# Kernel optimization log

Hardware: AMD Instinct MI355X
Metric: run time of the kernel (lower is better)

Reference implementation:

```python
import jax, jax.numpy as jnp
import numpy as np

B, S, H = 4, 1024, 2048
E = 16            # num_experts
K = 2             # num_experts_per_token
I = 1024          # per-expert intermediate_dim
N_SHARED = 2
I_SHARED = I * N_SHARED
RATIO = 0.1       # shared_expert_ratio
EPS = 1e-9


def _swiglu(x, wg, wu, wd):
    # SwiGLU, bias=False: down( silu(gate(x)) * up(x) )
    return (jax.nn.silu(x @ wg) * (x @ wu)) @ wd


def setup_inputs() -> dict:
    key = jax.random.key(0)
    ks = jax.random.split(key, 9)
    scale = 0.02
    x = jax.random.normal(ks[0], (B, S, H), dtype=jnp.float32)
    centroids = jax.random.normal(ks[1], (E, H), dtype=jnp.float32)  # nn.Parameter(randn)
    gate_bias = jnp.zeros((E,), dtype=jnp.float32)
    # shared expert SwiGLU weights (intermediate = I * n_shared_experts)
    wg_s = jax.random.normal(ks[2], (H, I_SHARED), dtype=jnp.float32) * scale
    wu_s = jax.random.normal(ks[3], (H, I_SHARED), dtype=jnp.float32) * scale
    wd_s = jax.random.normal(ks[4], (I_SHARED, H), dtype=jnp.float32) * scale
    # routed experts, stacked [E, ...]
    wg = jax.random.normal(ks[5], (E, H, I), dtype=jnp.float32) * scale
    wu = jax.random.normal(ks[6], (E, H, I), dtype=jnp.float32) * scale
    wd = jax.random.normal(ks[7], (E, I, H), dtype=jnp.float32) * scale
    return {"x": x, "centroids": centroids, "gate_bias": gate_bias,
            "wg_s": wg_s, "wu_s": wu_s, "wd_s": wd_s,
            "wg": wg, "wu": wu, "wd": wd}


def reference(x, centroids, gate_bias, wg_s, wu_s, wd_s, wg, wu, wd):
    # 1) shared expert on ALL tokens, scaled by ratio
    shared = _swiglu(x, wg_s, wu_s, wd_s) * RATIO          # [B,S,H]
    # 2) centroid affinity (DeepSeek-V3 sigmoid gating)
    affinity = jax.nn.sigmoid(jnp.einsum('bsh,eh->bse', x, centroids))  # [B,S,E]
    # 3) bias used ONLY for selection
    biased = affinity + gate_bias
    _, top_idx = jax.lax.top_k(biased, K)                  # [B,S,K]
    # 4) clean weights from unbiased affinity, normalized to sum 1
    top_aff = jnp.take_along_axis(affinity, top_idx, axis=-1)  # [B,S,K]
    weights = top_aff / (top_aff.sum(-1, keepdims=True) + EPS)
    # 5) combine-mask: per-token per-expert weight (0 if not selected)
    mask = (jax.nn.one_hot(top_idx, E, dtype=x.dtype) * weights[..., None]).sum(-2)  # [B,S,E]
    # 6) expert compute + weighted combine; loop over fixed small E avoids
    #    materializing a [B,S,E,H] tensor
    routed = jnp.zeros_like(x)
    for e in range(E):
        routed = routed + mask[..., e:e + 1] * _swiglu(x, wg[e], wu[e], wd[e])
    return shared + routed
```

## Files before the change

kernel.cpp:

```cpp
#include <hip/hip_runtime.h>
#include <hip/hip_bf16.h>

typedef unsigned short u16;
typedef unsigned int u32;
typedef unsigned long long u64;
typedef __attribute__((ext_vector_type(8))) short short8;
typedef __attribute__((ext_vector_type(4))) float f32x4;

#define TOKENS 4096
#define HDIM 2048
#define NEXP 16
#define IDIM 1024
#define ISH 2048
#define NCHUNK 128

#define GUITEMS 1152
#define DITEMS 2048

#define AS1(p) ((const __attribute__((address_space(1))) u32*)(p))
#define AS3(p) ((__attribute__((address_space(3))) u32*)(p))

__device__ __forceinline__ u16 f2b(float f) {
    u32 u = __float_as_uint(f);
    u32 r = u + 0x7fffu + ((u >> 16) & 1u);
    return (u16)(r >> 16);
}

__device__ __forceinline__ int item_index(int bid) {
    int x = bid & 7, j = bid >> 3;
    return ((x + 8 * (j >> 4)) << 4) | (j & 15);
}

__global__ __launch_bounds__(256) void route_kernel(const float* __restrict__ x,
                                                    const float* __restrict__ cent,
                                                    const float* __restrict__ bias,
                                                    u16* __restrict__ xb,
                                                    int* __restrict__ top_e,
                                                    float* __restrict__ top_w) {
    __shared__ alignas(16) float cs[8 * 2048];
    int lane = threadIdx.x & 63;
    int wv = threadIdx.x >> 6;
    int t = blockIdx.x * 4 + wv;
    const float4* xp4 = (const float4*)(x + (size_t)t * HDIM);
    float4 xr[8];
#pragma unroll
    for (int i = 0; i < 8; i++) xr[i] = xp4[lane + 64 * i];
    u16* xbp = xb + (size_t)t * HDIM;
#pragma unroll
    for (int i = 0; i < 8; i++) {
        u32 lo = (u32)f2b(xr[i].x) | ((u32)f2b(xr[i].y) << 16);
        u32 hi = (u32)f2b(xr[i].z) | ((u32)f2b(xr[i].w) << 16);
        uint2 o = make_uint2(lo, hi);
        *(uint2*)(xbp + (size_t)(lane + 64 * i) * 4) = o;
    }
    float aff[16];
#pragma unroll
    for (int ph = 0; ph < 2; ph++) {
        if (ph) __syncthreads();
        const float* sbase = cent + (size_t)(ph * 8 + wv * 2) * HDIM;
        float* dbase = cs + (size_t)wv * 2 * HDIM;
#pragma unroll
        for (int i = 0; i < 16; i++) {
            __builtin_amdgcn_global_load_lds(AS1(sbase + i * 256 + lane * 4),
                                             AS3(dbase + i * 256), 16, 0, 0);
        }
        __syncthreads();
#pragma unroll
        for (int e = 0; e < 8; e++) {
            const float4* cp = (const float4*)cs + (size_t)e * 512;
            float s = 0.f;
#pragma unroll
            for (int i = 0; i < 8; i++) {
                float4 cv = cp[lane + 64 * i];
                s += xr[i].x * cv.x;
                s += xr[i].y * cv.y;
                s += xr[i].z * cv.z;
                s += xr[i].w * cv.w;
            }
#pragma unroll
            for (int off = 32; off > 0; off >>= 1) s += __shfl_xor(s, off, 64);
            aff[ph * 8 + e] = 1.f / (1.f + expf(-s));
        }
    }
    float b0 = -1e30f, b1 = -1e30f, a0 = 0.f, a1 = 0.f;
    int e0 = -1, e1 = -1;
#pragma unroll
    for (int e = 0; e < 16; e++) {
        float v = aff[e] + bias[e];
        if (v > b0) {
            b1 = b0; e1 = e0; a1 = a0;
            b0 = v; e0 = e; a0 = aff[e];
        } else if (v > b1) {
            b1 = v; e1 = e; a1 = aff[e];
        }
    }
    float inv = 1.f / (a0 + a1 + 1e-9f);
    if (lane == 0) {
        top_e[2 * t] = e0; top_w[2 * t] = a0 * inv;
        top_e[2 * t + 1] = e1; top_w[2 * t + 1] = a1 * inv;
    }
}

__global__ __launch_bounds__(1024) void build_kernel(
    const int* __restrict__ top_e, const float* __restrict__ top_w,
    int* __restrict__ counts, int* __restrict__ offsets, int* __restrict__ itemsGU,
    int* __restrict__ itemsD, int* __restrict__ list_tok, int* __restrict__ tok2slot) {
    __shared__ int cnt[NCHUNK][16];
    __shared__ int offs_s[16];
    __shared__ int totals[16];
    __shared__ int guPref[16], dPref[16];
    int tid = threadIdx.x;
    int lane = tid & 63, wv = tid >> 6;
    for (int i = tid; i < GUITEMS; i += 1024) itemsGU[i] = -1;
    for (int i = tid; i < DITEMS; i += 1024) itemsD[i] = -1;
    for (int c = wv; c < NCHUNK; c += 16) {
        int v = top_e[c * 64 + lane];
#pragma unroll
        for (int e = 0; e < 16; e++) {
            u64 m = __ballot(v == e);
            if (lane == 0) cnt[c][e] = (int)__popcll(m);
        }
    }
    __syncthreads();
    if (tid < 16) {
        int s = 0;
        for (int c = 0; c < NCHUNK; c++) s += cnt[c][tid];
        totals[tid] = s;
        counts[tid] = s;
    }
    __syncthreads();
    if (tid == 0) {
        int r = 0, g = 0, d = 0;
        for (int e = 0; e < 16; e++) {
            offs_s[e] = r;
            offsets[e] = r;
            r += totals[e];
            guPref[e] = g;
            g += ((totals[e] + 127) >> 7) * 8;
            dPref[e] = d;
            d += ((totals[e] + 255) >> 8) * 32;
        }
    }
    if (tid < 512) {
        int i = tid;
        int g = i >> 4, s = i & 15;
        int y0 = (g >> 3) << 2, m0 = (g & 7) << 2;
        itemsGU[i] = ((m0 + (s >> 2)) << 8) | (y0 + (s & 3));
    }
    if (tid < 512) {
        int i = tid;
        int g = i >> 4, s = i & 15;
        int y0 = (g >> 2) << 2, m0 = (g & 3) << 2;
        itemsD[i] = ((m0 + (s >> 2)) << 8) | (y0 + (s & 3));
    }
    __syncthreads();
    if (tid < 16) {
        int e = tid;
        int tA = (totals[e] + 127) >> 7;
        int p = 512 + guPref[e];
        for (int y0 = 0; y0 < 8; y0 += 4)
            for (int m = 0; m < tA; m++)
                for (int dy = 0; dy < 4; dy++)
                    itemsGU[p++] = (1 << 28) | (e << 20) | (m << 8) | (y0 + dy);
        int tB = (totals[e] + 255) >> 8;
        p = 512 + dPref[e];
        for (int y0 = 0; y0 < 32; y0 += 4)
            for (int m = 0; m < tB; m++)
                for (int dy = 0; dy < 4; dy++)
                    itemsD[p++] = (1 << 28) | (e << 20) | (m << 8) | (y0 + dy);
        int r = offs_s[e];
        for (int c = 0; c < NCHUNK; c++) {
            int v = cnt[c][e];
            cnt[c][e] = r;
            r += v;
        }
    }
    __syncthreads();
    for (int c = wv; c < NCHUNK; c += 16) {
        int i = c * 64 + lane;
        int v = top_e[i];
        int rank = 0;
#pragma unroll
        for (int e = 0; e < 16; e++) {
            u64 m = __ballot(v == e);
            if (v == e) rank = (int)__popcll(m & ((1ull << lane) - 1ull));
        }
        int slot = cnt[c][v] + rank;
        list_tok[slot] = i >> 1;
        tok2slot[i] = slot;
    }
}

__global__ __launch_bounds__(256) void conv_all_kernel(
    const float* __restrict__ wgs, const float* __restrict__ wus,
    const float* __restrict__ wds, const float* __restrict__ wg,
    const float* __restrict__ wu, const float* __restrict__ wd, u16* __restrict__ Wt_gs,
    u16* __restrict__ Wt_us, u16* __restrict__ Wt_ds, u16* __restrict__ Wt_g,
    u16* __restrict__ Wt_u, u16* __restrict__ Wt_d) {
    int id = blockIdx.x;
    const float* Wm;
    u16* Wtm;
    int K, N, nt, kc;
    if (id < 768) {
        K = 2048; N = 2048;
        int seg = id >> 8, r = id & 255;
        nt = r & 31; kc = r >> 5;
        if (seg == 0) { Wm = wgs; Wtm = Wt_gs; }
        else if (seg == 1) { Wm = wus; Wtm = Wt_us; }
        else { Wm = wds; Wtm = Wt_ds; }
    } else if (id < 4864) {
        K = 2048; N = 1024;
        int r = id - 768;
        int m = r >> 11;
        r &= 2047;
        int e = r >> 7;
        r &= 127;
        nt = r & 15; kc = r >> 4;
        size_t off = (size_t)e * 2048 * 1024;
        if (m == 0) { Wm = wg + off; Wtm = Wt_g + off; }
        else { Wm = wu + off; Wtm = Wt_u + off; }
    } else {
        K = 1024; N = 2048;
        int r = id - 4864;
        int e = r >> 7;
        r &= 127;
        nt = r & 31; kc = r >> 5;
        size_t off = (size_t)e * 1024 * 2048;
        Wm = wd + off; Wtm = Wt_d + off;
    }
    int ksB = K >> 5;
    __shared__ u16 Ls[64 * 40];
    int t = threadIdx.x;
    int kr = t >> 3, ng = t & 7;
    int nn = t >> 2, seg2 = t & 3;
    int g = seg2 ^ ((nn >> 2) & 3);
#pragma unroll
    for (int s = 0; s < 8; s++) {
        int kb = kc * 256 + s * 32;
        const float* src = Wm + (size_t)(kb + kr) * N + nt * 64 + ng * 8;
        float4 f0 = *(const float4*)src;
        float4 f1 = *(const float4*)(src + 4);
        __syncthreads();
        const float* p0 = (const float*)&f0;
        const float* p1 = (const float*)&f1;
#pragma unroll
        for (int l = 0; l < 4; l++) Ls[(8 * ng + l) * 40 + kr] = f2b(p0[l]);
#pragma unroll
        for (int l = 0; l < 4; l++) Ls[(8 * ng + 4 + l) * 40 + kr] = f2b(p1[l]);
        __syncthreads();
        const u16* lp = &Ls[nn * 40 + g * 8];
        u32 w0 = (u32)lp[0] | ((u32)lp[1] << 16);
        u32 w1 = (u32)lp[2] | ((u32)lp[3] << 16);
        u32 w2 = (u32)lp[4] | ((u32)lp[5] << 16);
        u32 w3 = (u32)lp[6] | ((u32)lp[7] << 16);
        uint4 o = make_uint4(w0, w1, w2, w3);
        *(uint4*)(Wtm + (size_t)(nt * ksB + (kb >> 5)) * 2048 + t * 8) = o;
    }
}

__global__ __launch_bounds__(512, 4) void gemm_gateup(
    const u16* __restrict__ A, const u16* __restrict__ BgS, const u16* __restrict__ BuS,
    const u16* __restrict__ BgR, const u16* __restrict__ BuR, u16* __restrict__ hS,
    u16* __restrict__ hR, const int* __restrict__ counts, const int* __restrict__ offsets,
    const int* __restrict__ list_tok, const int* __restrict__ items) {
    int it = items[item_index(blockIdx.x)];
    if (it < 0) return;
    int routed = (it >> 28) & 1;
    int e = (it >> 20) & 15;
    int m0 = ((it >> 8) & 4095) * 128;
    int yb = it & 255;
    int cnt, base, Nout;
    u16* hout;
    const u16 *BgBase, *BuBase;
    if (routed) {
        cnt = counts[e];
        base = offsets[e];
        Nout = IDIM;
        size_t off = (size_t)e * HDIM * IDIM;
        BgBase = BgR + off;
        BuBase = BuR + off;
        hout = hR;
    } else {
        cnt = TOKENS;
        base = 0;
        Nout = ISH;
        BgBase = BgS;
        BuBase = BuS;
        hout = hS;
    }
    const int nk = HDIM >> 6;
    __shared__ alignas(16) u16 smem[24576];
    u16* As = smem;
    u16* Bgs = smem + 8192;
    u16* Bus = smem + 16384;
    float* us = (float*)smem;
    int tid = threadIdx.x;
    int lane = tid & 63, wv = tid >> 6;
    int wl = wv & 3, mat = wv >> 2;
    int quad = lane >> 4, mr = lane & 15;
    int gk = (tid & 3) ^ ((tid >> 4) & 3);
    int mg0 = min(m0 + (tid >> 2), cnt - 1);
    size_t sr0 = routed ? (size_t)list_tok[base + mg0] : (size_t)mg0;
    const u16* ap0 = A + sr0 * HDIM + gk * 8;
    size_t bstr = (size_t)(HDIM >> 5) * 2048;
    int t4 = tid & 255;
    const u16* Bsel = mat ? BuBase : BgBase;
    const u16* bsrc0 = Bsel + (size_t)(2 * yb) * bstr + (size_t)t4 * 8;
    const u16* bsrc1 = bsrc0 + bstr;
    u16* bb = mat ? Bus : Bgs;
    u16* bdst = bb + wl * 512;
    u16* adst = As + wv * 512;
    int xq = quad ^ ((mr >> 2) & 3);
    f32x4 acc[2][8];
#pragma unroll
    for (int i = 0; i < 2; i++)
#pragma unroll
        for (int j = 0; j < 8; j++) acc[i][j] = (f32x4)0.f;

    for (int ks = 0; ks < nk; ks++) {
        __syncthreads();
        __builtin_amdgcn_global_load_lds(AS1(ap0), AS3(adst), 16, 0, 0);
        __builtin_amdgcn_global_load_lds(AS1(ap0 + 32), AS3(adst + 4096), 16, 0, 0);
        __builtin_amdgcn_global_load_lds(AS1(bsrc0), AS3(bdst), 16, 0, 0);
        __builtin_amdgcn_global_load_lds(AS1(bsrc0 + 2048), AS3(bdst + 2048), 16, 0, 0);
        __builtin_amdgcn_global_load_lds(AS1(bsrc1), AS3(bdst + 4096), 16, 0, 0);
        __builtin_amdgcn_global_load_lds(AS1(bsrc1 + 2048), AS3(bdst + 6144), 16, 0, 0);
        ap0 += 64;
        bsrc0 += 4096;
        bsrc1 += 4096;
        __syncthreads();
#pragma unroll
        for (int c = 0; c < 2; c++) {
            short8 a0 = *(const short8*)(As + c * 4096 + ((32 * wl + mr) * 4 + xq) * 8);
            short8 a1 = *(const short8*)(As + c * 4096 + ((32 * wl + 16 + mr) * 4 + xq) * 8);
#pragma unroll
            for (int j = 0; j < 8; j++) {
                int h = j >> 2, jj = j & 3;
                short8 b = *(const short8*)(bb + h * 4096 + c * 2048 +
                                            (64 * jj + mr * 4 + xq) * 8);
                acc[0][j] = __builtin_amdgcn_mfma_f32_16x16x32_bf16(a0, b, acc[0][j], 0, 0, 0);
                acc[1][j] = __builtin_amdgcn_mfma_f32_16x16x32_bf16(a1, b, acc[1][j], 0, 0, 0);
            }
        }
    }
#pragma unroll
    for (int p = 0; p < 2; p++) {
        __syncthreads();
        if (mat == 1) {
#pragma unroll
            for (int i = 0; i < 2; i++)
#pragma unroll
                for (int jj = 0; jj < 4; jj++)
#pragma unroll
                    for (int r = 0; r < 4; r++) {
                        int row = 32 * wl + 16 * i + quad * 4 + r;
                        us[row * 64 + 16 * jj + mr] = acc[i][4 * p + jj][r];
                    }
        }
        __syncthreads();
        if (mat == 0) {
#pragma unroll
            for (int i = 0; i < 2; i++)
#pragma unroll
                for (int jj = 0; jj < 4; jj++)
#pragma unroll
                    for (int r = 0; r < 4; r++) {
                        int row = 32 * wl + 16 * i + quad * 4 + r;
                        int m = m0 + row;
                        if (m < cnt) {
                            float gv = acc[i][4 * p + jj][r];
                            float uv = us[row * 64 + 16 * jj + mr];
                            float h = gv / (1.f + expf(-gv)) * uv;
                            int n = yb * 128 + p * 64 + 16 * jj + mr;
                            hout[(size_t)(base + m) * Nout + n] = f2b(h);
                        }
                    }
        }
    }
}

__global__ __launch_bounds__(256) void gemm_down(
    const u16* __restrict__ hS, const u16* __restrict__ hR, const u16* __restrict__ BdS,
    const u16* __restrict__ BdR, float* __restrict__ out, float* __restrict__ rd,
    const int* __restrict__ counts, const int* __restrict__ offsets,
    const int* __restrict__ items) {
    int it = items[item_index(blockIdx.x)];
    if (it < 0) return;
    int routed = (it >> 28) & 1;
    int e = (it >> 20) & 15;
    int m0 = ((it >> 8) & 4095) * 256;
    int yb = it & 255;
    int cnt, base, Kd;
    const u16 *A, *B;
    float* outp;
    if (routed) {
        cnt = counts[e];
        base = offsets[e];
        Kd = IDIM;
        A = hR;
        B = BdR + (size_t)e * IDIM * HDIM;
        outp = rd;
    } else {
        cnt = TOKENS;
        base = 0;
        Kd = ISH;
        A = hS;
        B = BdS;
        outp = out;
    }
    int nk = Kd >> 6;
    __shared__ alignas(16) u16 As[256 * 64];
    __shared__ alignas(16) u16 Bs[64 * 64];
    int tid = threadIdx.x;
    int lane = tid & 63, wv = tid >> 6;
    int quad = lane >> 4, mr = lane & 15;
    int n0 = yb * 64;
    int gk = (tid & 3) ^ ((tid >> 4) & 3);
    const u16* ap0;
    const u16* ap1;
    const u16* ap2;
    const u16* ap3;
    {
        int mg0 = base + min(m0 + 0 * 64 + (tid >> 2), cnt - 1);
        int mg1 = base + min(m0 + 1 * 64 + (tid >> 2), cnt - 1);
        int mg2 = base + min(m0 + 2 * 64 + (tid >> 2), cnt - 1);
        int mg3 = base + min(m0 + 3 * 64 + (tid >> 2), cnt - 1);
        ap0 = A + (size_t)mg0 * Kd + gk * 8;
        ap1 = A + (size_t)mg1 * Kd + gk * 8;
        ap2 = A + (size_t)mg2 * Kd + gk * 8;
        ap3 = A + (size_t)mg3 * Kd + gk * 8;
    }
    size_t bstr = (size_t)(Kd >> 5) * 2048;
    const u16* bp = B + (size_t)yb * bstr + tid * 8;
    int xq = quad ^ ((mr >> 2) & 3);
    f32x4 acc[4][4];
#pragma unroll
    for (int i = 0; i < 4; i++)
#pragma unroll
        for (int j = 0; j < 4; j++) acc[i][j] = (f32x4)0.f;

    for (int ks = 0; ks < nk; ks++) {
        __syncthreads();
        __builtin_amdgcn_global_load_lds(AS1(ap0), AS3(As + 0 + wv * 512), 16, 0, 0);
        __builtin_amdgcn_global_load_lds(AS1(ap0 + 32), AS3(As + 8192 + wv * 512), 16, 0, 0);
        __builtin_amdgcn_global_load_lds(AS1(ap1), AS3(As + 2048 + wv * 512), 16, 0, 0);
        __builtin_amdgcn_global_load_lds(AS1(ap1 + 32), AS3(As + 10240 + wv * 512), 16, 0, 0);
        __builtin_amdgcn_global_load_lds(AS1(ap2), AS3(As + 4096 + wv * 512), 16, 0, 0);
        __builtin_amdgcn_global_load_lds(AS1(ap2 + 32), AS3(As + 12288 + wv * 512), 16, 0, 0);
        __builtin_amdgcn_global_load_lds(AS1(ap3), AS3(As + 6144 + wv * 512), 16, 0, 0);
        __builtin_amdgcn_global_load_lds(AS1(ap3 + 32), AS3(As + 14336 + wv * 512), 16, 0, 0);
        __builtin_amdgcn_global_load_lds(AS1(bp), AS3(Bs + wv * 512), 16, 0, 0);
        __builtin_amdgcn_global_load_lds(AS1(bp + 2048), AS3(Bs + 2048 + wv * 512), 16, 0, 0);
        ap0 += 64; ap1 += 64; ap2 += 64; ap3 += 64; bp += 4096;
        __syncthreads();
#pragma unroll
        for (int c = 0; c < 2; c++) {
            short8 a0 = *(const short8*)(As + c * 8192 + ((64 * wv + 0 + mr) * 4 + xq) * 8);
            short8 a1 = *(const short8*)(As + c * 8192 + ((64 * wv + 16 + mr) * 4 + xq) * 8);
            short8 a2 = *(const short8*)(As + c * 8192 + ((64 * wv + 32 + mr) * 4 + xq) * 8);
            short8 a3 = *(const short8*)(As + c * 8192 + ((64 * wv + 48 + mr) * 4 + xq) * 8);
#pragma unroll
            for (int j = 0; j < 4; j++) {
                short8 b = *(const short8*)(Bs + c * 2048 + (64 * j + mr * 4 + xq) * 8);
                acc[0][j] = __builtin_amdgcn_mfma_f32_16x16x32_bf16(a0, b, acc[0][j], 0, 0, 0);
                acc[1][j] = __builtin_amdgcn_mfma_f32_16x16x32_bf16(a1, b, acc[1][j], 0, 0, 0);
                acc[2][j] = __builtin_amdgcn_mfma_f32_16x16x32_bf16(a2, b, acc[2][j], 0, 0, 0);
                acc[3][j] = __builtin_amdgcn_mfma_f32_16x16x32_bf16(a3, b, acc[3][j], 0, 0, 0);
            }
        }
    }

#pragma unroll
    for (int i = 0; i < 4; i++)
#pragma unroll
        for (int j = 0; j < 4; j++)
#pragma unroll
            for (int r = 0; r < 4; r++) {
                int m = m0 + 64 * wv + 16 * i + quad * 4 + r;
                if (m >= cnt) continue;
                int n = n0 + 16 * j + mr;
                float v = acc[i][j][r];
                if (routed) {
                    outp[(size_t)(base + m) * HDIM + n] = v;
                } else {
                    outp[(size_t)m * HDIM + n] = 0.1f * v;
                }
            }
}

__global__ __launch_bounds__(256) void combine_kernel(float* __restrict__ out,
                                                      const float* __restrict__ rd,
                                                      const int* __restrict__ tok2slot,
                                                      const float* __restrict__ top_w) {
    int t = blockIdx.x;
    int s0 = tok2slot[2 * t], s1 = tok2slot[2 * t + 1];
    float w0 = top_w[2 * t], w1 = top_w[2 * t + 1];
    const float4* r0 = (const float4*)(rd + (size_t)s0 * HDIM);
    const float4* r1 = (const float4*)(rd + (size_t)s1 * HDIM);
    float4* op = (float4*)(out + (size_t)t * HDIM);
#pragma unroll
    for (int k = 0; k < 2; k++) {
        int c = threadIdx.x + k * 256;
        float4 o = op[c];
        float4 a = r0[c];
        float4 b = r1[c];
        o.x += w0 * a.x + w1 * b.x;
        o.y += w0 * a.y + w1 * b.y;
        o.z += w0 * a.z + w1 * b.z;
        o.w += w0 * a.w + w1 * b.w;
        op[c] = o;
    }
}

extern "C" void kernel_launch(void* const* d_in, const int* in_sizes, int n_in,
                              void* d_out, int out_size, void* d_ws, size_t ws_size,
                              hipStream_t stream) {
    const float* x = (const float*)d_in[0];
    const float* cent = (const float*)d_in[1];
    const float* bias = (const float*)d_in[2];
    const float* wgs = (const float*)d_in[3];
    const float* wus = (const float*)d_in[4];
    const float* wds = (const float*)d_in[5];
    const float* wg = (const float*)d_in[6];
    const float* wu = (const float*)d_in[7];
    const float* wd = (const float*)d_in[8];
    float* out = (float*)d_out;
    char* ws = (char*)d_ws;

    size_t off_wtgs = 0;
    size_t off_wtus = off_wtgs + (size_t)HDIM * ISH * 2;
    size_t off_wtds = off_wtus + (size_t)HDIM * ISH * 2;
    size_t off_wtg = off_wtds + (size_t)ISH * HDIM * 2;
    size_t off_wtu = off_wtg + (size_t)NEXP * HDIM * IDIM * 2;
    size_t off_wtd = off_wtu + (size_t)NEXP * HDIM * IDIM * 2;
    size_t off_xbf = off_wtd + (size_t)NEXP * IDIM * HDIM * 2;
    size_t off_hsh = off_xbf + (size_t)TOKENS * HDIM * 2;
    size_t off_hrt = off_hsh + (size_t)TOKENS * ISH * 2;
    size_t off_meta = off_hrt + (size_t)2 * TOKENS * IDIM * 2;
    size_t need = off_meta + (1 << 20);
    if (ws_size < need) return;

    u16* Wt_gs = (u16*)(ws + off_wtgs);
    u16* Wt_us = (u16*)(ws + off_wtus);
    u16* Wt_ds = (u16*)(ws + off_wtds);
    u16* Wt_g = (u16*)(ws + off_wtg);
    u16* Wt_u = (u16*)(ws + off_wtu);
    u16* Wt_d = (u16*)(ws + off_wtd);
    u16* x_bf = (u16*)(ws + off_xbf);
    u16* h_sh = (u16*)(ws + off_hsh);
    u16* h_rt = (u16*)(ws + off_hrt);
    float* rd = (float*)(ws + off_wtg);
    int* counts = (int*)(ws + off_meta);
    int* offsets = counts + 16;
    int* itemsGU = offsets + 16;
    int* itemsD = itemsGU + GUITEMS;
    int* tok2slot = itemsD + DITEMS;
    int* top_e = tok2slot + 2 * TOKENS;
    float* top_w = (float*)(top_e + 2 * TOKENS);
    int* list_tok = (int*)(top_w + 2 * TOKENS);

    route_kernel<<<TOKENS / 4, 256, 0, stream>>>(x, cent, bias, x_bf, top_e, top_w);
    build_kernel<<<1, 1024, 0, stream>>>(top_e, top_w, counts, offsets, itemsGU, itemsD,
                                         list_tok, tok2slot);
    conv_all_kernel<<<6912, 256, 0, stream>>>(wgs, wus, wds, wg, wu, wd, Wt_gs, Wt_us,
                                              Wt_ds, Wt_g, Wt_u, Wt_d);
    gemm_gateup<<<GUITEMS, 512, 0, stream>>>(x_bf, Wt_gs, Wt_us, Wt_g, Wt_u, h_sh, h_rt,
                                             counts, offsets, list_tok, itemsGU);
    gemm_down<<<DITEMS, 256, 0, stream>>>(h_sh, h_rt, Wt_ds, Wt_d, out, rd, counts,
                                          offsets, itemsD);
    combine_kernel<<<TOKENS, 256, 0, stream>>>(out, rd, tok2slot, top_w);
}
```

Before: 835.3 us.

## Triple-buffer gate/up GEMM LDS tiles with async prefetch and split-phase barriers

Replaces the single-buffered load-then-compute loop in gemm_gateup with a three-stage LDS ring that prefetches two k-steps ahead using global_load_lds. Loads for the next stage are interleaved between two MFMA half-phases, with vmcnt waits, raw s_barriers and s_setprio raised around the MFMA bursts. The aim is to hide global memory latency behind matrix math. In exchange, LDS use triples to 144 KB per block and launch bounds drop from 4 to 2 blocks, which lowers occupancy.

```diff
diff --git a/kernel.cpp b/kernel.cpp
--- a/kernel.cpp
+++ b/kernel.cpp
@@ -258,7 +258,7 @@
     }
 }
 
-__global__ __launch_bounds__(512, 4) void gemm_gateup(
+__global__ __launch_bounds__(512, 2) void gemm_gateup(
     const u16* __restrict__ A, const u16* __restrict__ BgS, const u16* __restrict__ BuS,
     const u16* __restrict__ BgR, const u16* __restrict__ BuR, u16* __restrict__ hS,
     u16* __restrict__ hR, const int* __restrict__ counts, const int* __restrict__ offsets,
@@ -289,10 +289,7 @@
         hout = hS;
     }
     const int nk = HDIM >> 6;
-    __shared__ alignas(16) u16 smem[24576];
-    u16* As = smem;
-    u16* Bgs = smem + 8192;
-    u16* Bus = smem + 16384;
+    __shared__ alignas(16) u16 smem[73728];
     float* us = (float*)smem;
     int tid = threadIdx.x;
     int lane = tid & 63, wv = tid >> 6;
@@ -307,42 +304,94 @@
     const u16* Bsel = mat ? BuBase : BgBase;
     const u16* bsrc0 = Bsel + (size_t)(2 * yb) * bstr + (size_t)t4 * 8;
     const u16* bsrc1 = bsrc0 + bstr;
-    u16* bb = mat ? Bus : Bgs;
-    u16* bdst = bb + wl * 512;
-    u16* adst = As + wv * 512;
+    const int matoff = mat ? 16384 : 8192;
     int xq = quad ^ ((mr >> 2) & 3);
+    int aoff0 = ((32 * wl + mr) * 4 + xq) * 8;
+    int aoff1 = ((32 * wl + 16 + mr) * 4 + xq) * 8;
     f32x4 acc[2][8];
 #pragma unroll
     for (int i = 0; i < 2; i++)
 #pragma unroll
         for (int j = 0; j < 8; j++) acc[i][j] = (f32x4)0.f;
 
+#define GLL(src, dstoff) \
+    __builtin_amdgcn_global_load_lds(AS1(src), AS3(smem + (dstoff)), 16, 0, 0)
+
+#pragma unroll
+    for (int b = 0; b < 2; b++) {
+        int bo = b * 24576;
+        GLL(ap0, bo + wv * 512);
+        GLL(ap0 + 32, bo + wv * 512 + 4096);
+        GLL(bsrc0, bo + matoff + wl * 512);
+        GLL(bsrc0 + 2048, bo + matoff + wl * 512 + 2048);
+        GLL(bsrc1, bo + matoff + wl * 512 + 4096);
+        GLL(bsrc1 + 2048, bo + matoff + wl * 512 + 6144);
+        ap0 += 64; bsrc0 += 4096; bsrc1 += 4096;
+    }
+    asm volatile("s_waitcnt vmcnt(6)" ::: "memory");
+    __builtin_amdgcn_s_barrier();
+
+    int curo = 0;
     for (int ks = 0; ks < nk; ks++) {
-        __syncthreads();
-        __builtin_amdgcn_global_load_lds(AS1(ap0), AS3(adst), 16, 0, 0);
-        __builtin_amdgcn_global_load_lds(AS1(ap0 + 32), AS3(adst + 4096), 16, 0, 0);
-        __builtin_amdgcn_global_load_lds(AS1(bsrc0), AS3(bdst), 16, 0, 0);
-        __builtin_amdgcn_global_load_lds(AS1(bsrc0 + 2048), AS3(bdst + 2048), 16, 0, 0);
-        __builtin_amdgcn_global_load_lds(AS1(bsrc1), AS3(bdst + 4096), 16, 0, 0);
-        __builtin_amdgcn_global_load_lds(AS1(bsrc1 + 2048), AS3(bdst + 6144), 16, 0, 0);
-        ap0 += 64;
-        bsrc0 += 4096;
-        bsrc1 += 4096;
-        __syncthreads();
-#pragma unroll
-        for (int c = 0; c < 2; c++) {
-            short8 a0 = *(const short8*)(As + c * 4096 + ((32 * wl + mr) * 4 + xq) * 8);
-            short8 a1 = *(const short8*)(As + c * 4096 + ((32 * wl + 16 + mr) * 4 + xq) * 8);
-#pragma unroll
-            for (int j = 0; j < 8; j++) {
-                int h = j >> 2, jj = j & 3;
-                short8 b = *(const short8*)(bb + h * 4096 + c * 2048 +
-                                            (64 * jj + mr * 4 + xq) * 8);
-                acc[0][j] = __builtin_amdgcn_mfma_f32_16x16x32_bf16(a0, b, acc[0][j], 0, 0, 0);
-                acc[1][j] = __builtin_amdgcn_mfma_f32_16x16x32_bf16(a1, b, acc[1][j], 0, 0, 0);
-            }
-        }
-    }
+        int n2o = curo + 49152;
+        if (n2o >= 73728) n2o -= 73728;
+        bool st = (ks + 2 < nk);
+        const u16* Asb = smem + curo;
+        const u16* bbb = smem + curo + matoff;
+        short8 a0 = *(const short8*)(Asb + aoff0);
+        short8 a1 = *(const short8*)(Asb + aoff1);
+        short8 bf[8];
+#pragma unroll
+        for (int j = 0; j < 8; j++)
+            bf[j] = *(const short8*)(bbb + (j >> 2) * 4096 +
+                                     (64 * (j & 3) + mr * 4 + xq) * 8);
+        if (st) {
+            GLL(ap0, n2o + wv * 512);
+            GLL(ap0 + 32, n2o + wv * 512 + 4096);
+            GLL(bsrc0, n2o + matoff + wl * 512);
+            ap0 += 64;
+        }
+        __builtin_amdgcn_s_barrier();
+        __builtin_amdgcn_s_setprio(1);
+#pragma unroll
+        for (int j = 0; j < 8; j++) {
+            acc[0][j] = __builtin_amdgcn_mfma_f32_16x16x32_bf16(a0, bf[j], acc[0][j], 0, 0, 0);
+            acc[1][j] = __builtin_amdgcn_mfma_f32_16x16x32_bf16(a1, bf[j], acc[1][j], 0, 0, 0);
+        }
+        __builtin_amdgcn_s_setprio(0);
+        __builtin_amdgcn_s_barrier();
+        a0 = *(const short8*)(Asb + 4096 + aoff0);
+        a1 = *(const short8*)(Asb + 4096 + aoff1);
+#pragma unroll
+        for (int j = 0; j < 8; j++)
+            bf[j] = *(const short8*)(bbb + (j >> 2) * 4096 + 2048 +
+                                     (64 * (j & 3) + mr * 4 + xq) * 8);
+        if (st) {
+            GLL(bsrc0 + 2048, n2o + matoff + wl * 512 + 2048);
+            GLL(bsrc1, n2o + matoff + wl * 512 + 4096);
+            GLL(bsrc1 + 2048, n2o + matoff + wl * 512 + 6144);
+            bsrc0 += 4096; bsrc1 += 4096;
+        }
+        if (ks + 1 < nk) {
+            if (st)
+                asm volatile("s_waitcnt vmcnt(6)" ::: "memory");
+            else
+                asm volatile("s_waitcnt vmcnt(0)" ::: "memory");
+        }
+        __builtin_amdgcn_s_barrier();
+        __builtin_amdgcn_s_setprio(1);
+#pragma unroll
+        for (int j = 0; j < 8; j++) {
+            acc[0][j] = __builtin_amdgcn_mfma_f32_16x16x32_bf16(a0, bf[j], acc[0][j], 0, 0, 0);
+            acc[1][j] = __builtin_amdgcn_mfma_f32_16x16x32_bf16(a1, bf[j], acc[1][j], 0, 0, 0);
+        }
+        __builtin_amdgcn_s_setprio(0);
+        __builtin_amdgcn_s_barrier();
+        curo += 24576;
+        if (curo >= 73728) curo = 0;
+    }
+#undef GLL
+
 #pragma unroll
     for (int p = 0; p < 2; p++) {
         __syncthreads();
```

After: 863.2 us. 3.3% more time.

## Widen down-projection GEMM tile to 256x128 with 512-thread blocks

Applied to the files above, without the earlier changes.

The down-projection GEMM now uses 512-thread blocks, each computing a 256x128 output tile instead of 256x64. Two wave groups share the same A tile in LDS and each takes one 64-column half of B. This halves the number of work items and the A-tile global reloads per output column. The cost is higher LDS use per block, fewer blocks to fill the CUs, and a rewritten work-item list in the build kernel.

```diff
diff --git a/kernel.cpp b/kernel.cpp
--- a/kernel.cpp
+++ b/kernel.cpp
@@ -15,7 +15,7 @@
 #define NCHUNK 128
 
 #define GUITEMS 1152
-#define DITEMS 2048
+#define DITEMS 1024
 
 #define AS1(p) ((const __attribute__((address_space(1))) u32*)(p))
 #define AS3(p) ((__attribute__((address_space(3))) u32*)(p))
@@ -138,7 +138,7 @@
             guPref[e] = g;
             g += ((totals[e] + 127) >> 7) * 8;
             dPref[e] = d;
-            d += ((totals[e] + 255) >> 8) * 32;
+            d += ((totals[e] + 255) >> 8) * 16;
         }
     }
     if (tid < 512) {
@@ -147,7 +147,7 @@
         int y0 = (g >> 3) << 2, m0 = (g & 7) << 2;
         itemsGU[i] = ((m0 + (s >> 2)) << 8) | (y0 + (s & 3));
     }
-    if (tid < 512) {
+    if (tid < 256) {
         int i = tid;
         int g = i >> 4, s = i & 15;
         int y0 = (g >> 2) << 2, m0 = (g & 3) << 2;
@@ -163,8 +163,8 @@
                 for (int dy = 0; dy < 4; dy++)
                     itemsGU[p++] = (1 << 28) | (e << 20) | (m << 8) | (y0 + dy);
         int tB = (totals[e] + 255) >> 8;
-        p = 512 + dPref[e];
-        for (int y0 = 0; y0 < 32; y0 += 4)
+        p = 256 + dPref[e];
+        for (int y0 = 0; y0 < 16; y0 += 4)
             for (int m = 0; m < tB; m++)
                 for (int dy = 0; dy < 4; dy++)
                     itemsD[p++] = (1 << 28) | (e << 20) | (m << 8) | (y0 + dy);
@@ -379,7 +379,7 @@
     }
 }
 
-__global__ __launch_bounds__(256) void gemm_down(
+__global__ __launch_bounds__(512, 4) void gemm_down(
     const u16* __restrict__ hS, const u16* __restrict__ hR, const u16* __restrict__ BdS,
     const u16* __restrict__ BdR, float* __restrict__ out, float* __restrict__ rd,
     const int* __restrict__ counts, const int* __restrict__ offsets,
@@ -409,29 +409,22 @@
         outp = out;
     }
     int nk = Kd >> 6;
-    __shared__ alignas(16) u16 As[256 * 64];
-    __shared__ alignas(16) u16 Bs[64 * 64];
+    __shared__ alignas(16) u16 As[2 * 8192];
+    __shared__ alignas(16) u16 Bs[2 * 4096];
     int tid = threadIdx.x;
     int lane = tid & 63, wv = tid >> 6;
+    int wl = wv & 3, nh = wv >> 2;
     int quad = lane >> 4, mr = lane & 15;
-    int n0 = yb * 64;
     int gk = (tid & 3) ^ ((tid >> 4) & 3);
-    const u16* ap0;
-    const u16* ap1;
-    const u16* ap2;
-    const u16* ap3;
-    {
-        int mg0 = base + min(m0 + 0 * 64 + (tid >> 2), cnt - 1);
-        int mg1 = base + min(m0 + 1 * 64 + (tid >> 2), cnt - 1);
-        int mg2 = base + min(m0 + 2 * 64 + (tid >> 2), cnt - 1);
-        int mg3 = base + min(m0 + 3 * 64 + (tid >> 2), cnt - 1);
-        ap0 = A + (size_t)mg0 * Kd + gk * 8;
-        ap1 = A + (size_t)mg1 * Kd + gk * 8;
-        ap2 = A + (size_t)mg2 * Kd + gk * 8;
-        ap3 = A + (size_t)mg3 * Kd + gk * 8;
-    }
+    int mg0 = base + min(m0 + (tid >> 2), cnt - 1);
+    int mg1 = base + min(m0 + 128 + (tid >> 2), cnt - 1);
+    const u16* ap0 = A + (size_t)mg0 * Kd + gk * 8;
+    const u16* ap1 = A + (size_t)mg1 * Kd + gk * 8;
     size_t bstr = (size_t)(Kd >> 5) * 2048;
-    const u16* bp = B + (size_t)yb * bstr + tid * 8;
+    int grp = tid >> 8;
+    int t4 = tid & 255;
+    const u16* bp = B + (size_t)(2 * yb + grp) * bstr + (size_t)t4 * 8;
+    u16* bdst = Bs + grp * 4096 + wl * 512;
     int xq = quad ^ ((mr >> 2) & 3);
     f32x4 acc[4][4];
 #pragma unroll
@@ -441,27 +434,24 @@
 
     for (int ks = 0; ks < nk; ks++) {
         __syncthreads();
-        __builtin_amdgcn_global_load_lds(AS1(ap0), AS3(As + 0 + wv * 512), 16, 0, 0);
+        __builtin_amdgcn_global_load_lds(AS1(ap0), AS3(As + wv * 512), 16, 0, 0);
         __builtin_amdgcn_global_load_lds(AS1(ap0 + 32), AS3(As + 8192 + wv * 512), 16, 0, 0);
-        __builtin_amdgcn_global_load_lds(AS1(ap1), AS3(As + 2048 + wv * 512), 16, 0, 0);
-        __builtin_amdgcn_global_load_lds(AS1(ap1 + 32), AS3(As + 10240 + wv * 512), 16, 0, 0);
-        __builtin_amdgcn_global_load_lds(AS1(ap2), AS3(As + 4096 + wv * 512), 16, 0, 0);
-        __builtin_amdgcn_global_load_lds(AS1(ap2 + 32), AS3(As + 12288 + wv * 512), 16, 0, 0);
-        __builtin_amdgcn_global_load_lds(AS1(ap3), AS3(As + 6144 + wv * 512), 16, 0, 0);
-        __builtin_amdgcn_global_load_lds(AS1(ap3 + 32), AS3(As + 14336 + wv * 512), 16, 0, 0);
-        __builtin_amdgcn_global_load_lds(AS1(bp), AS3(Bs + wv * 512), 16, 0, 0);
-        __builtin_amdgcn_global_load_lds(AS1(bp + 2048), AS3(Bs + 2048 + wv * 512), 16, 0, 0);
-        ap0 += 64; ap1 += 64; ap2 += 64; ap3 += 64; bp += 4096;
+        __builtin_amdgcn_global_load_lds(AS1(ap1), AS3(As + 4096 + wv * 512), 16, 0, 0);
+        __builtin_amdgcn_global_load_lds(AS1(ap1 + 32), AS3(As + 12288 + wv * 512), 16, 0, 0);
+        __builtin_amdgcn_global_load_lds(AS1(bp), AS3(bdst), 16, 0, 0);
+        __builtin_amdgcn_global_load_lds(AS1(bp + 2048), AS3(bdst + 2048), 16, 0, 0);
+        ap0 += 64; ap1 += 64; bp += 4096;
         __syncthreads();
 #pragma unroll
         for (int c = 0; c < 2; c++) {
-            short8 a0 = *(const short8*)(As + c * 8192 + ((64 * wv + 0 + mr) * 4 + xq) * 8);
-            short8 a1 = *(const short8*)(As + c * 8192 + ((64 * wv + 16 + mr) * 4 + xq) * 8);
-            short8 a2 = *(const short8*)(As + c * 8192 + ((64 * wv + 32 + mr) * 4 + xq) * 8);
-            short8 a3 = *(const short8*)(As + c * 8192 + ((64 * wv + 48 + mr) * 4 + xq) * 8);
+            short8 a0 = *(const short8*)(As + c * 8192 + ((64 * wl + 0 + mr) * 4 + xq) * 8);
+            short8 a1 = *(const short8*)(As + c * 8192 + ((64 * wl + 16 + mr) * 4 + xq) * 8);
+            short8 a2 = *(const short8*)(As + c * 8192 + ((64 * wl + 32 + mr) * 4 + xq) * 8);
+            short8 a3 = *(const short8*)(As + c * 8192 + ((64 * wl + 48 + mr) * 4 + xq) * 8);
 #pragma unroll
             for (int j = 0; j < 4; j++) {
-                short8 b = *(const short8*)(Bs + c * 2048 + (64 * j + mr * 4 + xq) * 8);
+                short8 b = *(const short8*)(Bs + nh * 4096 + c * 2048 +
+                                            (64 * j + mr * 4 + xq) * 8);
                 acc[0][j] = __builtin_amdgcn_mfma_f32_16x16x32_bf16(a0, b, acc[0][j], 0, 0, 0);
                 acc[1][j] = __builtin_amdgcn_mfma_f32_16x16x32_bf16(a1, b, acc[1][j], 0, 0, 0);
                 acc[2][j] = __builtin_amdgcn_mfma_f32_16x16x32_bf16(a2, b, acc[2][j], 0, 0, 0);
@@ -476,9 +466,9 @@
         for (int j = 0; j < 4; j++)
 #pragma unroll
             for (int r = 0; r < 4; r++) {
-                int m = m0 + 64 * wv + 16 * i + quad * 4 + r;
+                int m = m0 + 64 * wl + 16 * i + quad * 4 + r;
                 if (m >= cnt) continue;
-                int n = n0 + 16 * j + mr;
+                int n = yb * 128 + nh * 64 + 16 * j + mr;
                 float v = acc[i][j][r];
                 if (routed) {
                     outp[(size_t)(base + m) * HDIM + n] = v;
@@ -566,7 +556,7 @@
                                               Wt_ds, Wt_g, Wt_u, Wt_d);
     gemm_gateup<<<GUITEMS, 512, 0, stream>>>(x_bf, Wt_gs, Wt_us, Wt_g, Wt_u, h_sh, h_rt,
                                              counts, offsets, list_tok, itemsGU);
-    gemm_down<<<DITEMS, 256, 0, stream>>>(h_sh, h_rt, Wt_ds, Wt_d, out, rd, counts,
+    gemm_down<<<DITEMS, 512, 0, stream>>>(h_sh, h_rt, Wt_ds, Wt_d, out, rd, counts,
                                           offsets, itemsD);
     combine_kernel<<<TOKENS, 256, 0, stream>>>(out, rd, tok2slot, top_w);
 }
```

After: 819.7 us. No clear change (-1.9%).
